# Kernel tuning notes

Hardware: AMD Instinct MI355X
Metric: run time of the kernel (lower is better)

Reference implementation:

```python
import jax, jax.numpy as jnp
import numpy as np

B, T, D = 2, 8192, 1024
H = 4
QK = D // 2          # qk_dim = hidden_size * expand_qk
V = D                # value_dim = hidden_size
HK = QK // H         # head_qk_dim = 128
HV = V // H          # head_v_dim = 256
CHUNK = 16           # GLA chunk size (small to keep exp(+-cumsum(gk)) in fp32 range)
EPS = 1e-5


def setup_inputs() -> dict:
    key = jax.random.key(0)
    ks = jax.random.split(key, 9)
    s = 0.02
    hidden_states = jax.random.normal(ks[0], (B, T, D), jnp.float32)
    Wq = jax.random.normal(ks[1], (D, QK), jnp.float32) * s
    Wk = jax.random.normal(ks[2], (D, QK), jnp.float32) * s
    Wv = jax.random.normal(ks[3], (D, V), jnp.float32) * s
    Wa = jax.random.normal(ks[4], (D, H), jnp.float32) * s
    Wg = jax.random.normal(ks[5], (D, V), jnp.float32) * s
    Wo = jax.random.normal(ks[6], (V, D), jnp.float32) * s
    # A_log / dt_bias initialized exactly as in the torch module
    A = jax.random.uniform(ks[7], (H,), jnp.float32, 0.5, 16.0)
    A_log = jnp.log(A)
    dt = jnp.exp(jax.random.uniform(ks[8], (H,), jnp.float32)
                 * (np.log(0.1) - np.log(0.001)) + np.log(0.001))
    dt = jnp.clip(dt, 1e-4, None)
    dt_bias = dt + jnp.log(-jnp.expm1(-dt))   # inverse softplus of dt
    rms_w = jnp.ones((HV,), jnp.float32)
    return {"hidden_states": hidden_states, "Wq": Wq, "Wk": Wk, "Wv": Wv,
            "Wa": Wa, "Wg": Wg, "Wo": Wo, "A_log": A_log,
            "dt_bias": dt_bias, "rms_w": rms_w}


def _gla_forward(hidden_states, Wq, Wk, Wv, Wa, Wg, Wo, A_log, dt_bias, rms_w):
    q = hidden_states @ Wq
    k = hidden_states @ Wk
    v = hidden_states @ Wv
    alpha = hidden_states @ Wa                                   # [B,T,H]
    # mamba_decay: log-space gate, negative
    gk = -jnp.exp(A_log) * jax.nn.softplus(alpha + dt_bias)      # [B,T,H]

    qh = q.reshape(B, T, H, HK)
    kh = k.reshape(B, T, H, HK)
    vh = v.reshape(B, T, H, HV)
    gkh = jnp.broadcast_to(gk[..., None], (B, T, H, HK))

    Nc = T // CHUNK

    def chunks(x):  # [B,T,H,d] -> [Nc,B,H,C,d]
        return x.reshape(B, Nc, CHUNK, H, x.shape[-1]).transpose(1, 0, 3, 2, 4)

    qc, kc, vc, gc = chunks(qh), chunks(kh), chunks(vh), chunks(gkh)
    bcum = jnp.cumsum(gc, axis=-2)            # inclusive cumulative log-decay
    scale = HK ** -0.5                        # default scale in chunk_gla

    q_g = qc * jnp.exp(bcum) * scale          # [Nc,B,H,C,K]
    # intra-chunk causal scores: A_ij = q_i . (k_j * exp(b_i - b_j)), j <= i
    Ascore = jnp.einsum('nbhik,nbhjk->nbhij', q_g, kc * jnp.exp(-bcum))
    mask = jnp.tril(jnp.ones((CHUNK, CHUNK), bool))
    Ascore = jnp.where(mask, Ascore, 0.0)
    o_intra = jnp.einsum('nbhij,nbhjv->nbhiv', Ascore, vc)

    b_last = bcum[..., -1:, :]                # [Nc,B,H,1,K]
    k_out = kc * jnp.exp(b_last - bcum)       # keys decayed to chunk end

    def step(S, inp):
        qg, ko, vv, bl = inp                  # per-chunk slices
        o_inter = jnp.einsum('bhck,bhkv->bhcv', qg, S)
        S = jnp.exp(bl[..., 0, :])[..., None] * S \
            + jnp.einsum('bhck,bhcv->bhkv', ko, vv)
        return S, o_inter

    S0 = jnp.zeros((B, H, HK, HV), jnp.float32)
    _, o_inter = jax.lax.scan(step, S0, (q_g, k_out, vc, b_last))

    o = (o_intra + o_inter).transpose(1, 0, 3, 2, 4).reshape(B, T, H, HV)

    # fused per-head RMSNorm + swish output gate
    g = (hidden_states @ Wg).reshape(B, T, H, HV)
    o_n = o * jax.lax.rsqrt(jnp.mean(o * o, axis=-1, keepdims=True) + EPS) * rms_w
    o = o_n * (g * jax.nn.sigmoid(g))
    return o.reshape(B, T, V) @ Wo


def reference(hidden_states, Wq, Wk, Wv, Wa, Wg, Wo, A_log, dt_bias, rms_w):
    return _gla_forward(hidden_states, Wq, Wk, Wv, Wa, Wg, Wo,
                        A_log, dt_bias, rms_w)
```

## Files before the change

### kernel.cpp

```cpp
#include <hip/hip_runtime.h>
#include <cstdint>
#include <cstddef>

#define NB 2
#define NT 8192
#define ND 1024
#define NH 4
#define NV 1024
#define NHK 128
#define NHV 256
#define CHK 64
#define NCHK 128
#define QKS 1024
#define SCALE 0.08838834764831845f

using f32x4 = __attribute__((ext_vector_type(4))) float;
using short8 = __attribute__((ext_vector_type(8))) short;
using s16x4 = __attribute__((ext_vector_type(4))) short;

__device__ __forceinline__ float bf2f(unsigned short u){
  union { unsigned int i; float f; } t; t.i = ((unsigned int)u) << 16; return t.f;
}
__device__ __forceinline__ unsigned short f2bf(float f){
  union { float f; unsigned int i; } t; t.f = f;
  unsigned int r = t.i + 0x7fffu + ((t.i >> 16) & 1u);
  return (unsigned short)(r >> 16);
}
__device__ __forceinline__ double shfl_up_dbl(double v, int off){
  union { double d; unsigned int u[2]; } a, r;
  a.d = v;
  r.u[0] = __shfl_up(a.u[0], off, 64);
  r.u[1] = __shfl_up(a.u[1], off, 64);
  return r.d;
}
__device__ __forceinline__ void* lds_at(void* base, int row, int colElem, int rowBytes){
  return (void*)((char*)base + row*rowBytes + (((colElem*2) ^ ((row&7)<<4))));
}
__device__ __forceinline__ int osw(int rowl, int byteoff){
  return rowl*512 + (byteoff ^ (((rowl>>2)&7)<<4));
}

typedef const __attribute__((address_space(1))) unsigned int as1_u32;
typedef __attribute__((address_space(3))) unsigned int as3_u32;
__device__ __forceinline__ void gl_lds16(const void* g_lane, void* lds_uniform){
  __builtin_amdgcn_global_load_lds((as1_u32*)(uintptr_t)g_lane,
                                   (as3_u32*)(unsigned int)(uintptr_t)lds_uniform,
                                   16, 0, 0);
}

__global__ __launch_bounds__(256) void k_tc(const float* __restrict__ src,
                                            unsigned short* __restrict__ dst, int R, int C){
  int idx = blockIdx.x*256 + threadIdx.x;
  if (idx >= R*C) return;
  int r = idx % R, c = idx / R;
  dst[(size_t)c*R + r] = f2bf(src[(size_t)r*C + c]);
}

__global__ __launch_bounds__(256) void k_tc2(const float* __restrict__ src,
                                             unsigned short* __restrict__ dh,
                                             unsigned short* __restrict__ dl, int R, int C){
  int idx = blockIdx.x*256 + threadIdx.x;
  if (idx >= R*C) return;
  int r = idx % R, c = idx / R;
  float x = src[(size_t)r*C + c];
  unsigned short h = f2bf(x);
  unsigned short l = f2bf(x - bf2f(h));
  dh[(size_t)c*R + r] = h;
  dl[(size_t)c*R + r] = l;
}

__global__ __launch_bounds__(256) void k_alphacast(const float* __restrict__ hs,
                                                   const float* __restrict__ Wa,
                                                   const float* __restrict__ Al,
                                                   const float* __restrict__ dtb,
                                                   float* __restrict__ Gc,
                                                   unsigned short* __restrict__ hsh){
  int rowi = blockIdx.x;
  int tid = threadIdx.x;
  const float* h = hs + (size_t)rowi*ND;
  f32x4 x = *(const f32x4*)(h + tid*4);
  s16x4 hb;
  #pragma unroll
  for (int e=0;e<4;e++) hb[e] = (short)f2bf(x[e]);
  *(s16x4*)(hsh + (size_t)rowi*ND + tid*4) = hb;
  float a0=0.f,a1=0.f,a2=0.f,a3=0.f;
  #pragma unroll
  for (int e=0;e<4;e++){
    int d = tid*4+e;
    a0 += x[e]*Wa[d*4+0]; a1 += x[e]*Wa[d*4+1]; a2 += x[e]*Wa[d*4+2]; a3 += x[e]*Wa[d*4+3];
  }
  #pragma unroll
  for (int off=32; off>0; off>>=1){
    a0 += __shfl_down(a0, off, 64); a1 += __shfl_down(a1, off, 64);
    a2 += __shfl_down(a2, off, 64); a3 += __shfl_down(a3, off, 64);
  }
  __shared__ float red[4][4];
  if ((tid&63)==0){ int w = tid>>6; red[w][0]=a0; red[w][1]=a1; red[w][2]=a2; red[w][3]=a3; }
  __syncthreads();
  if (tid < 4){
    float al = red[0][tid]+red[1][tid]+red[2][tid]+red[3][tid];
    float xx = al + dtb[tid];
    float sp = (xx > 20.f) ? xx : log1pf(expf(xx));
    float gkv = -expf(Al[tid]) * sp;
    int bb = rowi >> 13, t = rowi & (NT-1);
    Gc[((size_t)(bb*NH + tid))*NT + t] = gkv;
  }
}

template<int BSPLIT, int GSWISH>
__global__ __launch_bounds__(256, BSPLIT ? 3 : 4)
void k_gemm2(const unsigned short* __restrict__ A2h,
             const unsigned short* __restrict__ Bth,
             const unsigned short* __restrict__ Btl,
             unsigned short* __restrict__ C, int M, int N, int K){
  __shared__ unsigned short sA[2][4096];
  __shared__ unsigned short sB[2][4096];
  __shared__ unsigned short sBl[2][4096];
  int tid = threadIdx.x, lane = tid & 63, wave = tid >> 6;
  int m0 = blockIdx.x*128, n0 = blockIdx.y*128;
  int wr = (wave>>1)*64, wc = (wave&1)*64;
  int row = lane & 15, kq = (lane>>4)*8;
  int rS = lane>>2, cS = (lane&3)*8;
  f32x4 acc[4][4];
  #pragma unroll
  for (int m=0;m<4;m++)
    #pragma unroll
    for (int n=0;n<4;n++)
      #pragma unroll
      for (int r=0;r<4;r++) acc[m][n][r] = 0.f;

  auto STAGE = [&](int buf, int k0){
    #pragma unroll
    for (int half=0; half<2; ++half){
      int rb = half*64 + wave*16;
      size_t gArow = (size_t)(m0 + rb + rS)*K + k0 + cS;
      size_t gBrow = (size_t)(n0 + rb + rS)*K + k0 + cS;
      gl_lds16(A2h + gArow, &sA[buf][rb*32]);
      gl_lds16(Bth + gBrow, &sB[buf][rb*32]);
      if (BSPLIT) gl_lds16(Btl + gBrow, &sBl[buf][rb*32]);
    }
  };

  STAGE(0, 0);
  __syncthreads();
  int nsteps = K >> 5;
  for (int t=0; t<nsteps; ++t){
    int cur = t & 1;
    if (t+1 < nsteps) STAGE(cur^1, (t+1)*32);
    short8 ah[4], bh[4];
    #pragma unroll
    for (int m=0;m<4;m++) ah[m] = *(const short8*)(&sA[cur][(wr + m*16 + row)*32 + kq]);
    #pragma unroll
    for (int n=0;n<4;n++) bh[n] = *(const short8*)(&sB[cur][(wc + n*16 + row)*32 + kq]);
    #pragma unroll
    for (int m=0;m<4;m++)
      #pragma unroll
      for (int n=0;n<4;n++)
        acc[m][n] = __builtin_amdgcn_mfma_f32_16x16x32_bf16(ah[m], bh[n], acc[m][n], 0, 0, 0);
    if (BSPLIT){
      short8 bl[4];
      #pragma unroll
      for (int n=0;n<4;n++) bl[n] = *(const short8*)(&sBl[cur][(wc + n*16 + row)*32 + kq]);
      #pragma unroll
      for (int m=0;m<4;m++)
        #pragma unroll
        for (int n=0;n<4;n++)
          acc[m][n] = __builtin_amdgcn_mfma_f32_16x16x32_bf16(ah[m], bl[n], acc[m][n], 0, 0, 0);
    }
    __syncthreads();
  }
  #pragma unroll
  for (int m=0;m<4;m++)
    #pragma unroll
    for (int n=0;n<4;n++)
      #pragma unroll
      for (int r=0;r<4;r++){
        int rr = m0 + wr + m*16 + (lane>>4)*4 + r;
        int cc = n0 + wc + n*16 + (lane&15);
        float v = acc[m][n][r];
        if (GSWISH) v = v / (1.f + expf(-v));
        C[(size_t)rr*N + cc] = f2bf(v);
      }
}

__global__ __launch_bounds__(256, 4) void k_gemm(const unsigned short* __restrict__ A,
                                                 const unsigned short* __restrict__ Bt,
                                                 float* __restrict__ C, int M, int N, int K){
  __shared__ unsigned short sA[2][4096];
  __shared__ unsigned short sB[2][4096];
  int tid = threadIdx.x, lane = tid & 63, wave = tid >> 6;
  int m0 = blockIdx.x*128, n0 = blockIdx.y*128;
  int wr = (wave>>1)*64, wc = (wave&1)*64;
  int row = lane & 15, kq = (lane>>4)*8;
  int rS = lane>>2, cS = (lane&3)*8;
  f32x4 acc[4][4];
  #pragma unroll
  for (int m=0;m<4;m++)
    #pragma unroll
    for (int n=0;n<4;n++)
      #pragma unroll
      for (int r=0;r<4;r++) acc[m][n][r] = 0.f;

  auto STAGE = [&](int buf, int k0){
    #pragma unroll
    for (int half=0; half<2; ++half){
      int rb = half*64 + wave*16;
      size_t gArow = (size_t)(m0 + rb + rS)*K + k0 + cS;
      size_t gBrow = (size_t)(n0 + rb + rS)*K + k0 + cS;
      gl_lds16(A  + gArow, &sA[buf][rb*32]);
      gl_lds16(Bt + gBrow, &sB[buf][rb*32]);
    }
  };

  STAGE(0, 0);
  __syncthreads();
  int nsteps = K >> 5;
  for (int t=0; t<nsteps; ++t){
    int cur = t & 1;
    if (t+1 < nsteps) STAGE(cur^1, (t+1)*32);
    short8 af[4], bfr[4];
    #pragma unroll
    for (int m=0;m<4;m++) af[m]  = *(const short8*)(&sA[cur][(wr + m*16 + row)*32 + kq]);
    #pragma unroll
    for (int n=0;n<4;n++) bfr[n] = *(const short8*)(&sB[cur][(wc + n*16 + row)*32 + kq]);
    #pragma unroll
    for (int m=0;m<4;m++)
      #pragma unroll
      for (int n=0;n<4;n++)
        acc[m][n] = __builtin_amdgcn_mfma_f32_16x16x32_bf16(af[m], bfr[n], acc[m][n], 0, 0, 0);
    __syncthreads();
  }
  #pragma unroll
  for (int m=0;m<4;m++)
    #pragma unroll
    for (int n=0;n<4;n++)
      #pragma unroll
      for (int r=0;r<4;r++){
        int rr = m0 + wr + m*16 + (lane>>4)*4 + r;
        int cc = n0 + wc + n*16 + (lane&15);
        C[(size_t)rr*N + cc] = acc[m][n][r];
      }
}

__global__ __launch_bounds__(256) void k_cumsum(const float* __restrict__ Gc, double* __restrict__ Gd){
  int bh = blockIdx.x, tid = threadIdx.x;
  const float* g = Gc + (size_t)bh*NT;
  double* out = Gd + (size_t)bh*NT;
  __shared__ double wsum[4];
  __shared__ double carry_s;
  if (tid==0) carry_s = 0.0;
  __syncthreads();
  for (int t0=0; t0<NT; t0+=256){
    double v = (double)g[t0+tid];
    #pragma unroll
    for (int off=1; off<64; off<<=1){
      double y = shfl_up_dbl(v, off);
      if ((tid&63) >= off) v += y;
    }
    if ((tid&63)==63) wsum[tid>>6] = v;
    __syncthreads();
    double add = carry_s;
    for (int w=0; w<(tid>>6); ++w) add += wsum[w];
    v += add;
    out[t0+tid] = v;
    __syncthreads();
    if (tid==255) carry_s = v;
    __syncthreads();
  }
}

__global__ __launch_bounds__(256, 2) void k_phaseA(const unsigned short* __restrict__ qkb,
                                                   const unsigned short* __restrict__ vb,
                                                   const double* __restrict__ Gd,
                                                   unsigned short* __restrict__ Sbc){
  __shared__ unsigned short vT[16384];
  __shared__ unsigned short wkT[8192];
  int blk = blockIdx.x, bh = blockIdx.y;
  int bb = bh>>2, hh = bh&3;
  int cs = blk*CHK, tid = threadIdx.x;
  int lane = tid & 63, w = tid >> 6;
  const double* Gb = Gd + (size_t)bh*NT;
  double Gend = Gb[cs + 63];
  #pragma unroll
  for (int it=0; it<8; ++it){
    int task = it*256 + tid;
    int j = task & 63, ng = task >> 6;
    short8 vv = *(const short8*)(vb + (size_t)(bb*NT + cs + j)*NV + hh*NHV + ng*8);
    #pragma unroll
    for (int e=0;e<8;e++)
      *(unsigned short*)lds_at(vT, ng*8+e, j, 128) = (unsigned short)vv[e];
  }
  #pragma unroll
  for (int it=0; it<4; ++it){
    int task = it*256 + tid;
    int j = task & 63, kg = task >> 6;
    float wj = expf((float)(Gend - Gb[cs + j]));
    short8 kv = *(const short8*)(qkb + (size_t)(bb*NT + cs + j)*QKS + 512 + hh*NHK + kg*8);
    #pragma unroll
    for (int e=0;e<8;e++)
      *(unsigned short*)lds_at(wkT, kg*8+e, j, 128) = f2bf(wj * bf2f((unsigned short)kv[e]));
  }
  __syncthreads();
  f32x4 sa[32];
  #pragma unroll
  for (int i=0;i<32;i++) sa[i] = (f32x4){0.f,0.f,0.f,0.f};
  short8 wa[2][2];
  #pragma unroll
  for (int mt=0;mt<2;mt++)
    #pragma unroll
    for (int kk=0;kk<2;kk++)
      wa[mt][kk] = *(short8*)lds_at(wkT, 32*w + mt*16 + (lane&15), kk*32 + (lane>>4)*8, 128);
  #pragma unroll
  for (int mt=0;mt<2;mt++)
    #pragma unroll
    for (int nt=0;nt<16;nt++)
      #pragma unroll
      for (int kk=0;kk<2;kk++){
        short8 b = *(short8*)lds_at(vT, nt*16 + (lane&15), kk*32 + (lane>>4)*8, 128);
        sa[mt*16+nt] = __builtin_amdgcn_mfma_f32_16x16x32_bf16(wa[mt][kk], b, sa[mt*16+nt], 0,0,0);
      }
  unsigned short* dst = Sbc + (size_t)(bh*NCHK + blk)*32768;
  #pragma unroll
  for (int mt=0;mt<2;mt++)
    #pragma unroll
    for (int nt=0;nt<16;nt++){
      int k = 32*w + mt*16 + (lane>>4)*4;
      int n = nt*16 + (lane&15);
      s16x4 p;
      #pragma unroll
      for (int r=0;r<4;r++) p[r] = (short)f2bf(sa[mt*16+nt][r]);
      *(s16x4*)(dst + (size_t)n*128 + k) = p;
    }
}

__global__ __launch_bounds__(256) void k_phaseB(unsigned short* __restrict__ Sbc,
                                                const double* __restrict__ Gd){
  int slice = blockIdx.x, bh = blockIdx.y;
  int tid = threadIdx.x;
  const double* Gb = Gd + (size_t)bh*NT;
  unsigned short* base = Sbc + (size_t)(bh*NCHK)*32768 + slice*1024 + tid*4;
  s16x4 c0 = *(const s16x4*)(base);
  f32x4 run;
  #pragma unroll
  for (int e=0;e<4;e++) run[e] = bf2f((unsigned short)c0[e]);
  s16x4 n0 = *(const s16x4*)(base + (size_t)1*32768);
  s16x4 n1 = *(const s16x4*)(base + (size_t)2*32768);
  s16x4 n2 = *(const s16x4*)(base + (size_t)3*32768);
  s16x4 n3 = *(const s16x4*)(base + (size_t)4*32768);
#define PB_STEP(U, BB) \
  { float resc = expf((float)(Gb[(BB)*CHK + 63] - Gb[(BB)*CHK - 1])); \
    s16x4 o_; \
    _Pragma("unroll") \
    for (int e=0;e<4;e++){ run[e] = resc*run[e] + bf2f((unsigned short)U[e]); o_[e] = (short)f2bf(run[e]); } \
    *(s16x4*)(base + (size_t)(BB)*32768) = o_; }
  for (int b=1; b<NCHK; b+=4){
    s16x4 u0=n0, u1=n1, u2=n2, u3=n3;
    if (b+4 < NCHK) n0 = *(const s16x4*)(base + (size_t)(b+4)*32768);
    if (b+5 < NCHK) n1 = *(const s16x4*)(base + (size_t)(b+5)*32768);
    if (b+6 < NCHK) n2 = *(const s16x4*)(base + (size_t)(b+6)*32768);
    if (b+7 < NCHK) n3 = *(const s16x4*)(base + (size_t)(b+7)*32768);
    PB_STEP(u0, b)
    if (b+1 < NCHK) PB_STEP(u1, b+1)
    if (b+2 < NCHK) PB_STEP(u2, b+2)
    if (b+3 < NCHK) PB_STEP(u3, b+3)
  }
#undef PB_STEP
}

__global__ __launch_bounds__(256, 3) void k_phaseC(const unsigned short* __restrict__ qkb,
                                                   const unsigned short* __restrict__ vb,
                                                   unsigned short* __restrict__ gio,
                                                   const float* __restrict__ rmsw,
                                                   const double* __restrict__ Gd,
                                                   const unsigned short* __restrict__ Sbc){
  __shared__ unsigned short vT[16384];
  __shared__ unsigned short scp[4096];
  __shared__ float Gsf[64];
  __shared__ float sI[64];
  __shared__ float rsum[64][4];
  __shared__ float frl[64];
  __shared__ float rms_s[256];
  int blk = blockIdx.x, bh = blockIdx.y;
  int bb = bh>>2, hh = bh&3;
  int cs = blk*CHK, tid = threadIdx.x;
  int lane = tid&63, w = tid>>6;
  const double* Gb = Gd + (size_t)bh*NT;
  rms_s[tid] = rmsw[tid];
  if (tid < 64){
    double ref = (cs == 0) ? 0.0 : Gb[cs-1];
    float g = (float)(Gb[cs+tid] - ref);
    Gsf[tid] = g;
    sI[tid] = SCALE * expf(g);
  }
  #pragma unroll
  for (int it=0; it<8; ++it){
    int task = it*256 + tid;
    int j = task & 63, ng = task >> 6;
    short8 vv = *(const short8*)(vb + (size_t)(bb*NT + cs + j)*NV + hh*NHV + ng*8);
    #pragma unroll
    for (int e=0;e<8;e++)
      *(unsigned short*)lds_at(vT, ng*8+e, j, 128) = (unsigned short)vv[e];
  }
  f32x4 oa[16];
  #pragma unroll
  for (int i=0;i<16;i++) oa[i] = (f32x4){0.f,0.f,0.f,0.f};
  if (blk > 0){
    const unsigned short* Sst = Sbc + (size_t)(bh*NCHK + blk - 1)*32768;
    #pragma unroll
    for (int kk=0;kk<4;kk++){
      short8 qrg[4];
      #pragma unroll
      for (int rg=0;rg<4;rg++)
        qrg[rg] = *(const short8*)(qkb + (size_t)(bb*NT + cs + rg*16 + (lane&15))*QKS
                                   + hh*NHK + kk*32 + (lane>>4)*8);
      #pragma unroll
      for (int nt=0;nt<4;nt++){
        short8 b = *(const short8*)(Sst + (size_t)(w*64 + nt*16 + (lane&15))*128
                                    + kk*32 + (lane>>4)*8);
        #pragma unroll
        for (int rg=0;rg<4;rg++)
          oa[rg*4+nt] = __builtin_amdgcn_mfma_f32_16x16x32_bf16(qrg[rg], b, oa[rg*4+nt], 0,0,0);
      }
    }
  }
  __syncthreads();
  if (blk > 0){
    #pragma unroll
    for (int rg=0;rg<4;rg++)
      #pragma unroll
      for (int r=0;r<4;r++){
        float srow = sI[rg*16 + (lane>>4)*4 + r];
        #pragma unroll
        for (int nt=0;nt<4;nt++) oa[rg*4+nt][r] *= srow;
      }
  }
  f32x4 pa[4];
  #pragma unroll
  for (int jt=0;jt<4;jt++) pa[jt] = (f32x4){0.f,0.f,0.f,0.f};
  {
    short8 qown[4];
    #pragma unroll
    for (int kk=0;kk<4;kk++)
      qown[kk] = *(const short8*)(qkb + (size_t)(bb*NT + cs + 16*w + (lane&15))*QKS
                                  + hh*NHK + kk*32 + (lane>>4)*8);
    #pragma unroll
    for (int jt=0;jt<4;jt++)
      #pragma unroll
      for (int kk=0;kk<4;kk++){
        short8 b = *(const short8*)(qkb + (size_t)(bb*NT + cs + jt*16 + (lane&15))*QKS
                                    + 512 + hh*NHK + kk*32 + (lane>>4)*8);
        pa[jt] = __builtin_amdgcn_mfma_f32_16x16x32_bf16(qown[kk], b, pa[jt], 0,0,0);
      }
  }
  #pragma unroll
  for (int jt=0;jt<4;jt++)
    #pragma unroll
    for (int r=0;r<4;r++){
      int il = 16*w + (lane>>4)*4 + r;
      int jl = jt*16 + (lane&15);
      float wgt = (jl <= il) ? SCALE * expf(Gsf[il] - Gsf[jl]) : 0.f;
      *(unsigned short*)lds_at(scp, il, jl, 128) = f2bf(wgt * pa[jt][r]);
    }
  __syncthreads();
  short8 af[4][2];
  #pragma unroll
  for (int rg=0;rg<4;rg++)
    #pragma unroll
    for (int kk=0;kk<2;kk++)
      af[rg][kk] = *(short8*)lds_at(scp, rg*16 + (lane&15), kk*32 + (lane>>4)*8, 128);
  #pragma unroll
  for (int nt=0;nt<4;nt++){
    short8 b0 = *(short8*)lds_at(vT, w*64 + nt*16 + (lane&15), 0*32 + (lane>>4)*8, 128);
    short8 b1 = *(short8*)lds_at(vT, w*64 + nt*16 + (lane&15), 1*32 + (lane>>4)*8, 128);
    #pragma unroll
    for (int rg=0;rg<4;rg++){
      oa[rg*4+nt] = __builtin_amdgcn_mfma_f32_16x16x32_bf16(af[rg][0], b0, oa[rg*4+nt], 0,0,0);
      oa[rg*4+nt] = __builtin_amdgcn_mfma_f32_16x16x32_bf16(af[rg][1], b1, oa[rg*4+nt], 0,0,0);
    }
  }
  float pp[16];
  #pragma unroll
  for (int rg=0;rg<4;rg++)
    #pragma unroll
    for (int r=0;r<4;r++){
      float s = 0.f;
      #pragma unroll
      for (int nt=0;nt<4;nt++) s += oa[rg*4+nt][r]*oa[rg*4+nt][r];
      pp[rg*4+r] = s;
    }
  #pragma unroll
  for (int i=0;i<16;i++){
    #pragma unroll
    for (int off=1; off<16; off<<=1) pp[i] += __shfl_xor(pp[i], off, 16);
  }
  if ((lane&15) == 0){
    int l4 = lane>>4;
    #pragma unroll
    for (int rg=0;rg<4;rg++)
      #pragma unroll
      for (int r=0;r<4;r++)
        rsum[rg*16 + l4*4 + r][w] = pp[rg*4+r];
  }
  __syncthreads();
  if (tid < 64)
    frl[tid] = rsqrtf((rsum[tid][0]+rsum[tid][1]+rsum[tid][2]+rsum[tid][3])*(1.f/256.f) + 1e-5f);
  __syncthreads();
  char* oLDS = (char*)vT;
  float fv[4][4];
  #pragma unroll
  for (int rg=0;rg<4;rg++)
    #pragma unroll
    for (int r=0;r<4;r++) fv[rg][r] = frl[rg*16 + (lane>>4)*4 + r];
  #pragma unroll
  for (int nt=0;nt<4;nt++){
    int n = w*64 + nt*16 + (lane&15);
    float rw = rms_s[n];
    #pragma unroll
    for (int rg=0;rg<4;rg++)
      #pragma unroll
      for (int r=0;r<4;r++){
        int rowl = rg*16 + (lane>>4)*4 + r;
        *(unsigned short*)(oLDS + osw(rowl, n*2)) = f2bf(oa[rg*4+nt][r] * fv[rg][r] * rw);
      }
  }
  __syncthreads();
  #pragma unroll
  for (int it=0; it<8; ++it){
    int task = it*256 + tid;
    int rowl = task >> 5, c8 = (task & 31)*8;
    size_t gbase = (size_t)(bb*NT + cs + rowl)*NV + hh*NHV + c8;
    short8 g8 = *(const short8*)(gio + gbase);
    short8 o8 = *(const short8*)(oLDS + osw(rowl, c8*2));
    short8 out;
    #pragma unroll
    for (int e=0;e<8;e++)
      out[e] = (short)f2bf(bf2f((unsigned short)o8[e]) * bf2f((unsigned short)g8[e]));
    *(short8*)(gio + gbase) = out;
  }
}

extern "C" void kernel_launch(void* const* d_in, const int* in_sizes, int n_in,
                              void* d_out, int out_size, void* d_ws, size_t ws_size,
                              hipStream_t stream) {
  (void)in_sizes; (void)n_in; (void)out_size;
  const float* hs  = (const float*)d_in[0];
  const float* Wq  = (const float*)d_in[1];
  const float* Wk  = (const float*)d_in[2];
  const float* Wv  = (const float*)d_in[3];
  const float* Wa  = (const float*)d_in[4];
  const float* Wg  = (const float*)d_in[5];
  const float* Wo  = (const float*)d_in[6];
  const float* Al  = (const float*)d_in[7];
  const float* dtb = (const float*)d_in[8];
  const float* rmsw= (const float*)d_in[9];
  char* ws = (char*)d_ws;

  constexpr size_t MB = 1048576;
  constexpr size_t OFF_QK   = 0;
  constexpr size_t OFF_V    = 32*MB;
  constexpr size_t OFF_G    = 64*MB;
  constexpr size_t OFF_WQKH = 96*MB;
  constexpr size_t OFF_WQKL = 98*MB;
  constexpr size_t OFF_WV   = 100*MB;
  constexpr size_t OFF_WG   = 102*MB;
  constexpr size_t OFF_WO   = 104*MB;
  constexpr size_t OFF_GC   = 106*MB;
  constexpr size_t OFF_GD   = 106*MB + 262144;
  constexpr size_t OFF_SBC  = 107*MB;
  constexpr size_t WS_REQUIRED = 176947200;
  if (ws_size < WS_REQUIRED) return;

  unsigned short* qkb  = (unsigned short*)(ws + OFF_QK);
  unsigned short* vb   = (unsigned short*)(ws + OFF_V);
  unsigned short* gb   = (unsigned short*)(ws + OFF_G);
  unsigned short* wqkh = (unsigned short*)(ws + OFF_WQKH);
  unsigned short* wqkl = (unsigned short*)(ws + OFF_WQKL);
  unsigned short* wvt  = (unsigned short*)(ws + OFF_WV);
  unsigned short* wgt  = (unsigned short*)(ws + OFF_WG);
  unsigned short* wot  = (unsigned short*)(ws + OFF_WO);
  float* Gc   = (float*)(ws + OFF_GC);
  double* Gd  = (double*)(ws + OFF_GD);
  unsigned short* Sbc = (unsigned short*)(ws + OFF_SBC);
  unsigned short* hsh = (unsigned short*)(ws + OFF_SBC);

  k_alphacast<<<16384, 256, 0, stream>>>(hs, Wa, Al, dtb, Gc, hsh);
  k_tc2<<<2048, 256, 0, stream>>>(Wq, wqkh, wqkl, 1024, 512);
  k_tc2<<<2048, 256, 0, stream>>>(Wk, wqkh + 512*1024, wqkl + 512*1024, 1024, 512);
  k_tc<<<4096, 256, 0, stream>>>(Wv, wvt, 1024, 1024);
  k_tc<<<4096, 256, 0, stream>>>(Wg, wgt, 1024, 1024);
  k_tc<<<4096, 256, 0, stream>>>(Wo, wot, 1024, 1024);

  k_gemm2<1,0><<<dim3(128,8), 256, 0, stream>>>(hsh, wqkh, wqkl, qkb, 16384, 1024, 1024);
  k_gemm2<0,0><<<dim3(128,8), 256, 0, stream>>>(hsh, wvt, nullptr, vb, 16384, 1024, 1024);
  k_gemm2<0,1><<<dim3(128,8), 256, 0, stream>>>(hsh, wgt, nullptr, gb, 16384, 1024, 1024);

  k_cumsum<<<8, 256, 0, stream>>>(Gc, Gd);

  k_phaseA<<<dim3(NCHK,8), 256, 0, stream>>>(qkb, vb, Gd, Sbc);
  k_phaseB<<<dim3(32,8), 256, 0, stream>>>(Sbc, Gd);
  k_phaseC<<<dim3(NCHK,8), 256, 0, stream>>>(qkb, vb, gb, rmsw, Gd, Sbc);

  k_gemm<<<dim3(128,8), 256, 0, stream>>>(gb, wot, (float*)d_out, 16384, 1024, 1024);
}
```

Baseline: 432.2 us.

## Replace V/G/O projection GEMMs with 256x256-tile 512-thread swizzled GEMM

Adds a new GEMM kernel with 256x256 output tiles, 8 waves, K-step 64, XOR-swizzled LDS layout, double-buffered direct global-to-LDS loads with explicit vmcnt waits, a grouped block-to-tile mapping, and s_setprio around the MFMA loop. It replaces the V projection, the gated-swish G projection and the output projection. Larger tiles raise arithmetic intensity per LDS byte and cut global reloads. The cost is 128KB of dynamic LDS per block, which limits occupancy. The gemm2 launch bound is also changed to 3.

```diff
diff --git a/kernel.cpp b/kernel.cpp
--- a/kernel.cpp
+++ b/kernel.cpp
@@ -108,7 +108,7 @@
 }
 
 template<int BSPLIT, int GSWISH>
-__global__ __launch_bounds__(256, BSPLIT ? 3 : 4)
+__global__ __launch_bounds__(256, 3)
 void k_gemm2(const unsigned short* __restrict__ A2h,
              const unsigned short* __restrict__ Bth,
              const unsigned short* __restrict__ Btl,
@@ -183,62 +183,85 @@
       }
 }
 
-__global__ __launch_bounds__(256, 4) void k_gemm(const unsigned short* __restrict__ A,
-                                                 const unsigned short* __restrict__ Bt,
-                                                 float* __restrict__ C, int M, int N, int K){
-  __shared__ unsigned short sA[2][4096];
-  __shared__ unsigned short sB[2][4096];
-  int tid = threadIdx.x, lane = tid & 63, wave = tid >> 6;
-  int m0 = blockIdx.x*128, n0 = blockIdx.y*128;
-  int wr = (wave>>1)*64, wc = (wave&1)*64;
-  int row = lane & 15, kq = (lane>>4)*8;
-  int rS = lane>>2, cS = (lane&3)*8;
-  f32x4 acc[4][4];
-  #pragma unroll
-  for (int m=0;m<4;m++)
+template<int GSWISH, typename OutT>
+__global__ __launch_bounds__(512, 2)
+void k_gemm8(const unsigned short* __restrict__ A,
+             const unsigned short* __restrict__ Bt,
+             OutT* __restrict__ C, int M, int N, int K){
+  extern __shared__ unsigned short sm8[];
+  int tid = threadIdx.x, lane = tid & 63, wv = tid >> 6;
+  int wm = wv >> 2, wn = wv & 3;
+  int flat = blockIdx.y*gridDim.x + blockIdx.x;
+  int cpx = (gridDim.x*gridDim.y) >> 3;
+  int wg = (flat & 7)*cpx + (flat >> 3);
+  int m0 = (wg % gridDim.x)*256, n0 = (wg / gridDim.x)*256;
+
+  f32x4 acc[8][4];
+  #pragma unroll
+  for (int m=0;m<8;m++)
     #pragma unroll
     for (int n=0;n<4;n++)
       #pragma unroll
       for (int r=0;r<4;r++) acc[m][n][r] = 0.f;
 
+  int srcOff = (((lane&7) ^ ((lane>>3)&7)))*8;
+  int rowInW = lane>>3;
   auto STAGE = [&](int buf, int k0){
-    #pragma unroll
-    for (int half=0; half<2; ++half){
-      int rb = half*64 + wave*16;
-      size_t gArow = (size_t)(m0 + rb + rS)*K + k0 + cS;
-      size_t gBrow = (size_t)(n0 + rb + rS)*K + k0 + cS;
-      gl_lds16(A  + gArow, &sA[buf][rb*32]);
-      gl_lds16(Bt + gBrow, &sB[buf][rb*32]);
+    unsigned short* dA = sm8 + buf*16384;
+    unsigned short* dB = sm8 + 32768 + buf*16384;
+    #pragma unroll
+    for (int i=0;i<4;i++){
+      int rb = i*64 + wv*8;
+      gl_lds16(A  + (size_t)(m0 + rb + rowInW)*K + k0 + srcOff, dA + rb*64);
+      gl_lds16(Bt + (size_t)(n0 + rb + rowInW)*K + k0 + srcOff, dB + rb*64);
     }
   };
 
   STAGE(0, 0);
-  __syncthreads();
-  int nsteps = K >> 5;
+  STAGE(1, 64);
+  int nsteps = K >> 6;
   for (int t=0; t<nsteps; ++t){
-    int cur = t & 1;
-    if (t+1 < nsteps) STAGE(cur^1, (t+1)*32);
-    short8 af[4], bfr[4];
-    #pragma unroll
-    for (int m=0;m<4;m++) af[m]  = *(const short8*)(&sA[cur][(wr + m*16 + row)*32 + kq]);
-    #pragma unroll
-    for (int n=0;n<4;n++) bfr[n] = *(const short8*)(&sB[cur][(wc + n*16 + row)*32 + kq]);
-    #pragma unroll
-    for (int m=0;m<4;m++)
+    unsigned short* cA = sm8 + (t&1)*16384;
+    unsigned short* cB = sm8 + 32768 + (t&1)*16384;
+    if (t+1 < nsteps) asm volatile("s_waitcnt vmcnt(8)" ::: "memory");
+    else              asm volatile("s_waitcnt vmcnt(0)" ::: "memory");
+    __builtin_amdgcn_s_barrier();
+    asm volatile("" ::: "memory");
+    __builtin_amdgcn_s_setprio(1);
+    #pragma unroll
+    for (int kk=0;kk<2;kk++){
+      int slot = ((kk*4 + (lane>>4)) ^ (lane&7))*8;
+      short8 am[8], bn[4];
+      #pragma unroll
+      for (int m=0;m<8;m++)
+        am[m] = *(const short8*)(cA + (wm*128 + m*16 + (lane&15))*64 + slot);
       #pragma unroll
       for (int n=0;n<4;n++)
-        acc[m][n] = __builtin_amdgcn_mfma_f32_16x16x32_bf16(af[m], bfr[n], acc[m][n], 0, 0, 0);
-    __syncthreads();
-  }
-  #pragma unroll
-  for (int m=0;m<4;m++)
+        bn[n] = *(const short8*)(cB + (wn*64 + n*16 + (lane&15))*64 + slot);
+      #pragma unroll
+      for (int m=0;m<8;m++)
+        #pragma unroll
+        for (int n=0;n<4;n++)
+          acc[m][n] = __builtin_amdgcn_mfma_f32_16x16x32_bf16(am[m], bn[n], acc[m][n], 0, 0, 0);
+    }
+    __builtin_amdgcn_s_setprio(0);
+    asm volatile("" ::: "memory");
+    __builtin_amdgcn_s_barrier();
+    asm volatile("" ::: "memory");
+    if (t+2 < nsteps) STAGE(t&1, (t+2)*64);
+  }
+  #pragma unroll
+  for (int m=0;m<8;m++)
     #pragma unroll
     for (int n=0;n<4;n++)
       #pragma unroll
       for (int r=0;r<4;r++){
-        int rr = m0 + wr + m*16 + (lane>>4)*4 + r;
-        int cc = n0 + wc + n*16 + (lane&15);
-        C[(size_t)rr*N + cc] = acc[m][n][r];
+        int rr = m0 + wm*128 + m*16 + (lane>>4)*4 + r;
+        int cc = n0 + wn*64 + n*16 + (lane&15);
+        float v = acc[m][n][r];
+        if (GSWISH) v = v / (1.f + expf(-v));
+        if (sizeof(OutT) == 2) C[(size_t)rr*N + cc] = (OutT)f2bf(v);
+        else                   C[(size_t)rr*N + cc] = (OutT)v;
       }
 }
 
@@ -590,9 +613,17 @@
   k_tc<<<4096, 256, 0, stream>>>(Wg, wgt, 1024, 1024);
   k_tc<<<4096, 256, 0, stream>>>(Wo, wot, 1024, 1024);
 
+  constexpr int LDS8 = 131072;
+  (void)hipFuncSetAttribute(reinterpret_cast<const void*>(k_gemm8<0, unsigned short>),
+                            hipFuncAttributeMaxDynamicSharedMemorySize, LDS8);
+  (void)hipFuncSetAttribute(reinterpret_cast<const void*>(k_gemm8<1, unsigned short>),
+                            hipFuncAttributeMaxDynamicSharedMemorySize, LDS8);
+  (void)hipFuncSetAttribute(reinterpret_cast<const void*>(k_gemm8<0, float>),
+                            hipFuncAttributeMaxDynamicSharedMemorySize, LDS8);
+
   k_gemm2<1,0><<<dim3(128,8), 256, 0, stream>>>(hsh, wqkh, wqkl, qkb, 16384, 1024, 1024);
-  k_gemm2<0,0><<<dim3(128,8), 256, 0, stream>>>(hsh, wvt, nullptr, vb, 16384, 1024, 1024);
-  k_gemm2<0,1><<<dim3(128,8), 256, 0, stream>>>(hsh, wgt, nullptr, gb, 16384, 1024, 1024);
+  k_gemm8<0, unsigned short><<<dim3(64,4), 512, LDS8, stream>>>(hsh, wvt, vb, 16384, 1024, 1024);
+  k_gemm8<1, unsigned short><<<dim3(64,4), 512, LDS8, stream>>>(hsh, wgt, gb, 16384, 1024, 1024);
 
   k_cumsum<<<8, 256, 0, stream>>>(Gc, Gd);
 
@@ -600,5 +631,5 @@
   k_phaseB<<<dim3(32,8), 256, 0, stream>>>(Sbc, Gd);
   k_phaseC<<<dim3(NCHK,8), 256, 0, stream>>>(qkb, vb, gb, rmsw, Gd, Sbc);
 
-  k_gemm<<<dim3(128,8), 256, 0, stream>>>(gb, wot, (float*)d_out, 16384, 1024, 1024);
-}
+  k_gemm8<0, float><<<dim3(64,4), 512, LDS8, stream>>>(gb, wot, (float*)d_out, 16384, 1024, 1024);
+}
```

Result: slower. 451.3 us (+4.4%).
